# Optimization experiments

Hardware: AMD Instinct MI355X
Metric: run time of the kernel (lower is better)

The kernel has to match this reference:

```python
import jax, jax.numpy as jnp
import numpy as np

N_HEAD = 16

def setup_inputs() -> dict:
    key = jax.random.key(0)
    k1, k2, k3 = jax.random.split(key, 3)
    B, T, C = 2, 2048, 2048
    x = jax.random.normal(k1, (B, T, C), dtype=jnp.float32)
    # torch Linear weights are [out, in]; init with small scale for stability
    w_attn = jax.random.normal(k2, (3 * C, C), dtype=jnp.float32) * 0.02
    b_attn = jnp.zeros((3 * C,), dtype=jnp.float32)
    w_proj = jax.random.normal(k3, (C, C), dtype=jnp.float32) * 0.02
    b_proj = jnp.zeros((C,), dtype=jnp.float32)
    return {"x": x, "w_attn": w_attn, "b_attn": b_attn, "w_proj": w_proj, "b_proj": b_proj}

def reference(x, w_attn, b_attn, w_proj, b_proj):
    B, T, C = x.shape
    nh = N_HEAD
    hs = C // nh
    # fused QKV projection (torch Linear: x @ W^T + b)
    qkv = x @ w_attn.T + b_attn                      # [B, T, 3C]
    q, k, v = jnp.split(qkv, 3, axis=2)
    # [B, nh, T, hs]
    q = q.reshape(B, T, nh, hs).transpose(0, 2, 1, 3)
    k = k.reshape(B, T, nh, hs).transpose(0, 2, 1, 3)
    v = v.reshape(B, T, nh, hs).transpose(0, 2, 1, 3)
    # causal scaled dot-product attention
    scale = 1.0 / jnp.sqrt(jnp.asarray(hs, dtype=x.dtype))
    logits = jnp.einsum("bhqd,bhkd->bhqk", q, k) * scale  # [B, nh, T, T]
    causal = jnp.tril(jnp.ones((T, T), dtype=bool))
    logits = jnp.where(causal, logits, jnp.finfo(logits.dtype).min)
    attn = jax.nn.softmax(logits, axis=-1)
    y = jnp.einsum("bhqk,bhkd->bhqd", attn, v)       # [B, nh, T, hs]
    y = y.transpose(0, 2, 1, 3).reshape(B, T, C)
    # output projection (resid_dropout is identity in eval / p=0)
    y = y @ w_proj.T + b_proj
    return y
```

## Files before the change

### kernel.cpp

```cpp
#include <hip/hip_runtime.h>
#include <stdint.h>

typedef __bf16 bf16_t;
typedef __bf16 bf16x8 __attribute__((ext_vector_type(8)));
typedef float f32x4 __attribute__((ext_vector_type(4)));
typedef unsigned short us16x8 __attribute__((ext_vector_type(8)));

#define MFMA16(a, b, c) __builtin_amdgcn_mfma_f32_16x16x32_bf16(a, b, c, 0, 0, 0)
#define BAR() __builtin_amdgcn_s_barrier()
#define PRIO1() __builtin_amdgcn_s_setprio(1)
#define PRIO0() __builtin_amdgcn_s_setprio(0)
#define LGKM0()                                        \
  do {                                                 \
    asm volatile("s_waitcnt lgkmcnt(0)" ::: "memory"); \
    __builtin_amdgcn_sched_barrier(0);                 \
  } while (0)
#define VMCNT(n)                                          \
  do {                                                    \
    asm volatile("s_waitcnt vmcnt(" #n ")" ::: "memory"); \
    __builtin_amdgcn_sched_barrier(0);                    \
  } while (0)

__device__ __forceinline__ void stage16(const bf16_t* g, bf16_t* l) {
  __builtin_amdgcn_global_load_lds((__attribute__((address_space(1))) void*)g,
                                   (__attribute__((address_space(3))) void*)l, 16, 0, 0);
}

__global__ __launch_bounds__(256) void cvt_f32_to_bf16(const float* __restrict__ in,
                                                       bf16_t* __restrict__ out, int n8) {
  int i = blockIdx.x * 256 + threadIdx.x;
  if (i >= n8) return;
  const f32x4* p = (const f32x4*)(in + (size_t)i * 8);
  f32x4 a = p[0], b = p[1];
  bf16x8 o;
  o[0] = (bf16_t)a[0]; o[1] = (bf16_t)a[1]; o[2] = (bf16_t)a[2]; o[3] = (bf16_t)a[3];
  o[4] = (bf16_t)b[0]; o[5] = (bf16_t)b[1]; o[6] = (bf16_t)b[2]; o[7] = (bf16_t)b[3];
  *(bf16x8*)(out + (size_t)i * 8) = o;
}

template <int OUT_BF16>
__global__ __launch_bounds__(256, 2) void gemm_w128p(const bf16_t* __restrict__ A,
                                                     const bf16_t* __restrict__ B,
                                                     const float* __restrict__ bias,
                                                     void* __restrict__ Cout,
                                                     int M, int N, int K) {
  __shared__ bf16_t SA[3 * 256 * 32];
  __shared__ bf16_t SB[3 * 128 * 32];
  const int tid = threadIdx.x;
  const int l = tid & 63, w = tid >> 6;
  const int l15 = l & 15, l4 = l >> 4;
  const int wm = w >> 1, wn = w & 1;
  const int nbn = N >> 7;
  const int nbm = M >> 8;
  const int total = nbm * nbn;
  const int bnpc = nbn >> 3;

  const int r0 = tid >> 2;
  const int scol = (((tid & 3) ^ ((r0 >> 1) & 3)) << 3);
  const size_t K64 = (size_t)64 * K;

  const int swz = (l4 ^ ((l15 >> 1) & 3)) << 3;
  int aoff[8], boff[4];
#pragma unroll
  for (int i = 0; i < 8; ++i) aoff[i] = (wm * 128 + i * 16 + l15) * 32 + swz;
#pragma unroll
  for (int i = 0; i < 4; ++i) boff[i] = (wn * 64 + i * 16 + l15) * 32 + swz;

  const int nk = K >> 5;

  for (int wk = blockIdx.x; wk < total; wk += gridDim.x) {
    const int c = wk & 7, rr0 = wk >> 3;
    const int bm = rr0 / bnpc;
    const int bn = c * bnpc + rr0 % bnpc;

    const bf16_t* gA = A + (size_t)(bm * 256 + r0) * K + scol;
    const bf16_t* gB = B + (size_t)(bn * 128 + r0) * K + scol;

    f32x4 acc[8][4] = {};

    auto STAGE = [&](int t2, int buf) {
      const size_t ko = (size_t)t2 * 32;
      stage16(gA + ko, SA + buf * 8192 + tid * 8);
      stage16(gA + K64 + ko, SA + buf * 8192 + 2048 + tid * 8);
      stage16(gA + 2 * K64 + ko, SA + buf * 8192 + 4096 + tid * 8);
      stage16(gA + 3 * K64 + ko, SA + buf * 8192 + 6144 + tid * 8);
      stage16(gB + ko, SB + buf * 4096 + tid * 8);
      stage16(gB + K64 + ko, SB + buf * 4096 + 2048 + tid * 8);
    };

    auto TILE = [&](int t, int bufR, int bufS) {
      const int t2 = (t + 2 < nk) ? t + 2 : nk - 1;
      STAGE(t2, bufS);
      bf16x8 aR[8], bR[4];
#pragma unroll
      for (int i = 0; i < 8; ++i) aR[i] = *(const bf16x8*)(SA + bufR * 8192 + aoff[i]);
#pragma unroll
      for (int i = 0; i < 4; ++i) bR[i] = *(const bf16x8*)(SB + bufR * 4096 + boff[i]);
      VMCNT(6);
      BAR();
      LGKM0();
      PRIO1();
#pragma unroll
      for (int mi = 0; mi < 8; ++mi)
#pragma unroll
        for (int ni = 0; ni < 4; ++ni)
          acc[mi][ni] = MFMA16(aR[mi], bR[ni], acc[mi][ni]);
      PRIO0();
      BAR();
    };

    STAGE(0, 0);
    STAGE(1, 1);
    VMCNT(6);
    BAR();

    for (int t = 0; t < nk - 1; t += 3) {
      TILE(t, 0, 2);
      TILE(t + 1, 1, 0);
      TILE(t + 2, 2, 1);
    }
    TILE(nk - 1, 0, 2);
    VMCNT(0);

    const int rbase = bm * 256 + wm * 128 + (l4 << 2);
    const int cbase = bn * 128 + wn * 64 + l15;
#pragma unroll
    for (int ni = 0; ni < 4; ++ni) {
      float bv = bias[cbase + ni * 16];
#pragma unroll
      for (int mi = 0; mi < 8; ++mi)
#pragma unroll
        for (int rr = 0; rr < 4; ++rr) {
          float v = acc[mi][ni][rr] + bv;
          size_t off = (size_t)(rbase + mi * 16 + rr) * N + (cbase + ni * 16);
          if (OUT_BF16) ((bf16_t*)Cout)[off] = (bf16_t)v;
          else ((float*)Cout)[off] = v;
        }
    }
  }
}

template <int OUT_BF16>
__global__ __launch_bounds__(256, 3) void gemm_tb3(const bf16_t* __restrict__ A,
                                                   const bf16_t* __restrict__ B,
                                                   const float* __restrict__ bias,
                                                   void* __restrict__ Cout,
                                                   int M, int N, int K) {
  __shared__ bf16_t SA[3 * 128 * 32];
  __shared__ bf16_t SB[3 * 128 * 32];
  const int tid = threadIdx.x;
  const int l = tid & 63, w = tid >> 6;
  const int l15 = l & 15, l4 = l >> 4;
  const int wm = w >> 1, wn = w & 1;
  const int nbm = M >> 7;
  const int nwg = gridDim.x;
  const int bid = blockIdx.x;
  const int wg = (bid & 7) * (nwg >> 3) + (bid >> 3);
  const int bn = wg / nbm, bm = wg % nbm;

  const int r0 = tid >> 2;
  const int sc = (((tid & 3) ^ ((r0 >> 1) & 3)) << 3);
  const bf16_t* gA = A + (size_t)(bm * 128 + r0) * K + sc;
  const bf16_t* gB = B + (size_t)(bn * 128 + r0) * K + sc;
  const size_t rowK64 = (size_t)64 * K;

  const int swz = (l4 ^ ((l15 >> 1) & 3)) << 3;
  int aoff[4], boff[4];
#pragma unroll
  for (int i = 0; i < 4; ++i) {
    aoff[i] = (wm * 64 + i * 16 + l15) * 32 + swz;
    boff[i] = (wn * 64 + i * 16 + l15) * 32 + swz;
  }

  f32x4 acc[4][4] = {};
  const int nk = K >> 5;

  auto STAGE = [&](int t2, int buf) {
    const size_t ko = (size_t)t2 * 32;
    stage16(gA + ko, SA + buf * 4096 + tid * 8);
    stage16(gA + rowK64 + ko, SA + buf * 4096 + 2048 + tid * 8);
    stage16(gB + ko, SB + buf * 4096 + tid * 8);
    stage16(gB + rowK64 + ko, SB + buf * 4096 + 2048 + tid * 8);
  };

  auto TILE = [&](int t, int bufR, int bufS) {
    const int t2 = (t + 2 < nk) ? t + 2 : nk - 1;
    STAGE(t2, bufS);
    bf16x8 aR[4], bR[4];
#pragma unroll
    for (int i = 0; i < 4; ++i) {
      aR[i] = *(const bf16x8*)(SA + bufR * 4096 + aoff[i]);
      bR[i] = *(const bf16x8*)(SB + bufR * 4096 + boff[i]);
    }
    VMCNT(4);
    BAR();
    LGKM0();
    PRIO1();
#pragma unroll
    for (int mi = 0; mi < 4; ++mi)
#pragma unroll
      for (int ni = 0; ni < 4; ++ni)
        acc[mi][ni] = MFMA16(aR[mi], bR[ni], acc[mi][ni]);
    PRIO0();
    BAR();
  };

  STAGE(0, 0);
  STAGE(1, 1);
  VMCNT(4);
  BAR();

  for (int t = 0; t < nk - 1; t += 3) {
    TILE(t, 0, 2);
    TILE(t + 1, 1, 0);
    TILE(t + 2, 2, 1);
  }
  TILE(nk - 1, 0, 2);
  VMCNT(0);

  const int rbase = bm * 128 + wm * 64 + (l4 << 2);
  const int cbase = bn * 128 + wn * 64 + l15;
#pragma unroll
  for (int ni = 0; ni < 4; ++ni) {
    float bv = bias[cbase + ni * 16];
#pragma unroll
    for (int mi = 0; mi < 4; ++mi)
#pragma unroll
      for (int r = 0; r < 4; ++r) {
        float v = acc[mi][ni][r] + bv;
        size_t off = (size_t)(rbase + mi * 16 + r) * N + (cbase + ni * 16);
        if (OUT_BF16) ((bf16_t*)Cout)[off] = (bf16_t)v;
        else ((float*)Cout)[off] = v;
      }
  }
}

__global__ __launch_bounds__(256, 2) void attn_fwd(const bf16_t* __restrict__ qkv,
                                                   bf16_t* __restrict__ att) {
  __shared__ bf16_t Kt[64 * 128];
  __shared__ bf16_t Vt[128 * 64];
  __shared__ bf16_t Pw[4][16 * 64];

  int bid = blockIdx.x;
  int pair = bid >> 5, bh = bid & 31;
  int h = bh & 15, b = bh >> 4;
  int tid = threadIdx.x;
  int l = tid & 63, w = tid >> 6;
  int l15 = l & 15, l4 = l >> 4, l7 = l & 7;
  const size_t LD = 6144;
  const bf16_t* base = qkv + (size_t)b * 2048 * LD;

#pragma unroll 1
  for (int phase = 0; phase < 2; ++phase) {
    int qt = phase ? 31 - pair : pair;
    int q0 = qt << 6;
    int wq0 = q0 + w * 16;

    bf16x8 qf[4];
#pragma unroll
    for (int kk = 0; kk < 4; ++kk)
      qf[kk] = *(const bf16x8*)(base + (size_t)(wq0 + l15) * LD + h * 128 + kk * 32 + l4 * 8);

    f32x4 acc[8] = {};
    float mrow[4], lrow[4];
#pragma unroll
    for (int r = 0; r < 4; ++r) { mrow[r] = -1e30f; lrow[r] = 0.f; }

    int nkt = qt + 1;
    for (int kt = 0; kt < nkt; ++kt) {
      int kb = kt << 6;
      const bf16_t* vg = base + (size_t)kb * LD + 4096 + h * 128;
      us16x8 va[2], vb[2];
#pragma unroll
      for (int p = 0; p < 2; ++p) {
        int g = p * 256 + tid;
        int kv = (g >> 4) << 1;
        int d0 = (g & 15) << 3;
        va[p] = *(const us16x8*)(vg + (size_t)kv * LD + d0);
        vb[p] = *(const us16x8*)(vg + (size_t)(kv + 1) * LD + d0);
      }
      const bf16_t* kg = base + (size_t)kb * LD + 2048 + h * 128;
#pragma unroll
      for (int i = 0; i < 4; ++i) {
        int e = i * 256 + tid;
        int row = e >> 4, blk = e & 15;
        int src = (blk ^ (row & 7)) << 3;
        stage16(kg + (size_t)row * LD + src, Kt + e * 8);
      }
#pragma unroll
      for (int p = 0; p < 2; ++p) {
        int g = p * 256 + tid;
        int kv = (g >> 4) << 1;
        int d0 = (g & 15) << 3;
        int k8 = kv >> 3, kr = kv & 7;
#pragma unroll
        for (int j = 0; j < 8; ++j) {
          int d = d0 + j;
          int swz = k8 ^ ((d ^ (d >> 3)) & 7);
          unsigned pack = (unsigned)va[p][j] | ((unsigned)vb[p][j] << 16);
          *(unsigned*)(&Vt[d * 64 + swz * 8 + kr]) = pack;
        }
      }
      __syncthreads();

      {
        f32x4 s[4] = {};
        __builtin_amdgcn_s_setprio(1);
#pragma unroll
        for (int kk = 0; kk < 4; ++kk) {
          int blk = (kk * 4 + l4) ^ l7;
#pragma unroll
          for (int n = 0; n < 4; ++n) {
            bf16x8 kf = *(const bf16x8*)(Kt + (n * 16 + l15) * 128 + blk * 8);
            s[n] = MFMA16(qf[kk], kf, s[n]);
          }
        }
        __builtin_amdgcn_s_setprio(0);

        const float sc = 0.08838834764831845f;
        bool needMask = (kb + 63) > wq0;
        float scf[4];
#pragma unroll
        for (int r = 0; r < 4; ++r) {
          int q = wq0 + (l4 << 2) + r;
#pragma unroll
          for (int n = 0; n < 4; ++n) {
            float v = s[n][r] * sc;
            if (needMask && (kb + n * 16 + l15) > q) v = -1e30f;
            s[n][r] = v;
          }
          float mx = fmaxf(fmaxf(s[0][r], s[1][r]), fmaxf(s[2][r], s[3][r]));
          mx = fmaxf(mx, __shfl_xor(mx, 1));
          mx = fmaxf(mx, __shfl_xor(mx, 2));
          mx = fmaxf(mx, __shfl_xor(mx, 4));
          mx = fmaxf(mx, __shfl_xor(mx, 8));
          float mn = fmaxf(mrow[r], mx);
          float sf = __expf(mrow[r] - mn);
          mrow[r] = mn;
          scf[r] = sf;
          float rs = 0.f;
#pragma unroll
          for (int n = 0; n < 4; ++n) {
            float pv = __expf(s[n][r] - mn);
            s[n][r] = pv;
            rs += pv;
          }
          rs += __shfl_xor(rs, 1);
          rs += __shfl_xor(rs, 2);
          rs += __shfl_xor(rs, 4);
          rs += __shfl_xor(rs, 8);
          lrow[r] = lrow[r] * sf + rs;
        }
#pragma unroll
        for (int nd = 0; nd < 8; ++nd)
#pragma unroll
          for (int r = 0; r < 4; ++r)
            acc[nd][r] *= scf[r];
#pragma unroll
        for (int n = 0; n < 4; ++n) {
          int cb8 = n * 2 + (l15 >> 3);
#pragma unroll
          for (int r = 0; r < 4; ++r) {
            int row = (l4 << 2) + r;
            Pw[w][row * 64 + ((cb8 ^ (row & 7)) << 3) + l7] = (bf16_t)s[n][r];
          }
        }
        __builtin_amdgcn_s_setprio(1);
#pragma unroll
        for (int kk2 = 0; kk2 < 2; ++kk2) {
          bf16x8 pa = *(const bf16x8*)(&Pw[w][l15 * 64 + (((kk2 * 4 + l4) ^ l7) << 3)]);
#pragma unroll
          for (int nd = 0; nd < 8; ++nd) {
            int d = nd * 16 + l15;
            int swz = (kk2 * 4 + l4) ^ ((d ^ (d >> 3)) & 7);
            bf16x8 bv = *(const bf16x8*)(&Vt[d * 64 + swz * 8]);
            acc[nd] = MFMA16(pa, bv, acc[nd]);
          }
        }
        __builtin_amdgcn_s_setprio(0);
      }
      __syncthreads();
    }

#pragma unroll
    for (int r = 0; r < 4; ++r) {
      float inv = 1.0f / lrow[r];
      size_t ro = (size_t)(b * 2048 + wq0 + (l4 << 2) + r) * 2048 + h * 128;
#pragma unroll
      for (int nd = 0; nd < 8; ++nd)
        att[ro + nd * 16 + l15] = (bf16_t)(acc[nd][r] * inv);
    }
  }
}

extern "C" void kernel_launch(void* const* d_in, const int* in_sizes, int n_in,
                              void* d_out, int out_size, void* d_ws, size_t ws_size,
                              hipStream_t stream) {
  (void)in_sizes; (void)n_in; (void)out_size; (void)ws_size;
  const float* x = (const float*)d_in[0];
  const float* w_attn = (const float*)d_in[1];
  const float* b_attn = (const float*)d_in[2];
  const float* w_proj = (const float*)d_in[3];
  const float* b_proj = (const float*)d_in[4];
  float* out = (float*)d_out;

  char* ws = (char*)d_ws;
  bf16_t* xb  = (bf16_t*)(ws);
  bf16_t* wab = (bf16_t*)(ws + 16777216);
  bf16_t* wpb = (bf16_t*)(ws + 41943040);
  bf16_t* qkv = (bf16_t*)(ws + 50331648);
  bf16_t* att = xb;

  cvt_f32_to_bf16<<<4096, 256, 0, stream>>>(x, xb, 1048576);
  cvt_f32_to_bf16<<<6144, 256, 0, stream>>>(w_attn, wab, 1572864);
  cvt_f32_to_bf16<<<2048, 256, 0, stream>>>(w_proj, wpb, 524288);

  gemm_w128p<1><<<512, 256, 0, stream>>>(xb, wab, b_attn, qkv, 4096, 6144, 2048);

  attn_fwd<<<512, 256, 0, stream>>>(qkv, att);

  gemm_tb3<0><<<512, 256, 0, stream>>>(att, wpb, b_proj, out, 4096, 2048, 2048);
}
```

Baseline: 286.7 us.

## Double-buffer K/V tiles in attention, merge conversions, reuse wide GEMM for projection

Attention now double-buffers the K and V shared-memory tiles. The next tile's global loads are issued before the current tile's QK and PV math, which hides load latency and leaves one barrier per iteration. The three f32-to-bf16 conversion launches are merged into one kernel. The output projection now uses the 256x128-tile GEMM with 256 blocks instead of the removed 128x128 kernel. Doubling the K/V buffers raises LDS use and may cut attention occupancy, and the projection GEMM with 256 blocks may underfill the GPU.

New measurement: 296.9 us. 1.04x slower.

```diff
diff --git a/kernel.cpp b/kernel.cpp
--- a/kernel.cpp
+++ b/kernel.cpp
@@ -26,16 +26,33 @@
                                    (__attribute__((address_space(3))) void*)l, 16, 0, 0);
 }
 
-__global__ __launch_bounds__(256) void cvt_f32_to_bf16(const float* __restrict__ in,
-                                                       bf16_t* __restrict__ out, int n8) {
+__global__ __launch_bounds__(256) void cvt_all(const float* __restrict__ x,
+                                               const float* __restrict__ wa,
+                                               const float* __restrict__ wp,
+                                               bf16_t* __restrict__ xb,
+                                               bf16_t* __restrict__ wab,
+                                               bf16_t* __restrict__ wpb) {
   int i = blockIdx.x * 256 + threadIdx.x;
-  if (i >= n8) return;
-  const f32x4* p = (const f32x4*)(in + (size_t)i * 8);
+  const float* src;
+  bf16_t* dst;
+  if (i < 1048576) {
+    src = x + (size_t)i * 8;
+    dst = xb + (size_t)i * 8;
+  } else if (i < 2621440) {
+    size_t j = (size_t)(i - 1048576) * 8;
+    src = wa + j;
+    dst = wab + j;
+  } else {
+    size_t j = (size_t)(i - 2621440) * 8;
+    src = wp + j;
+    dst = wpb + j;
+  }
+  const f32x4* p = (const f32x4*)src;
   f32x4 a = p[0], b = p[1];
   bf16x8 o;
   o[0] = (bf16_t)a[0]; o[1] = (bf16_t)a[1]; o[2] = (bf16_t)a[2]; o[3] = (bf16_t)a[3];
   o[4] = (bf16_t)b[0]; o[5] = (bf16_t)b[1]; o[6] = (bf16_t)b[2]; o[7] = (bf16_t)b[3];
-  *(bf16x8*)(out + (size_t)i * 8) = o;
+  *(bf16x8*)dst = o;
 }
 
 template <int OUT_BF16>
@@ -140,105 +157,10 @@
   }
 }
 
-template <int OUT_BF16>
-__global__ __launch_bounds__(256, 3) void gemm_tb3(const bf16_t* __restrict__ A,
-                                                   const bf16_t* __restrict__ B,
-                                                   const float* __restrict__ bias,
-                                                   void* __restrict__ Cout,
-                                                   int M, int N, int K) {
-  __shared__ bf16_t SA[3 * 128 * 32];
-  __shared__ bf16_t SB[3 * 128 * 32];
-  const int tid = threadIdx.x;
-  const int l = tid & 63, w = tid >> 6;
-  const int l15 = l & 15, l4 = l >> 4;
-  const int wm = w >> 1, wn = w & 1;
-  const int nbm = M >> 7;
-  const int nwg = gridDim.x;
-  const int bid = blockIdx.x;
-  const int wg = (bid & 7) * (nwg >> 3) + (bid >> 3);
-  const int bn = wg / nbm, bm = wg % nbm;
-
-  const int r0 = tid >> 2;
-  const int sc = (((tid & 3) ^ ((r0 >> 1) & 3)) << 3);
-  const bf16_t* gA = A + (size_t)(bm * 128 + r0) * K + sc;
-  const bf16_t* gB = B + (size_t)(bn * 128 + r0) * K + sc;
-  const size_t rowK64 = (size_t)64 * K;
-
-  const int swz = (l4 ^ ((l15 >> 1) & 3)) << 3;
-  int aoff[4], boff[4];
-#pragma unroll
-  for (int i = 0; i < 4; ++i) {
-    aoff[i] = (wm * 64 + i * 16 + l15) * 32 + swz;
-    boff[i] = (wn * 64 + i * 16 + l15) * 32 + swz;
-  }
-
-  f32x4 acc[4][4] = {};
-  const int nk = K >> 5;
-
-  auto STAGE = [&](int t2, int buf) {
-    const size_t ko = (size_t)t2 * 32;
-    stage16(gA + ko, SA + buf * 4096 + tid * 8);
-    stage16(gA + rowK64 + ko, SA + buf * 4096 + 2048 + tid * 8);
-    stage16(gB + ko, SB + buf * 4096 + tid * 8);
-    stage16(gB + rowK64 + ko, SB + buf * 4096 + 2048 + tid * 8);
-  };
-
-  auto TILE = [&](int t, int bufR, int bufS) {
-    const int t2 = (t + 2 < nk) ? t + 2 : nk - 1;
-    STAGE(t2, bufS);
-    bf16x8 aR[4], bR[4];
-#pragma unroll
-    for (int i = 0; i < 4; ++i) {
-      aR[i] = *(const bf16x8*)(SA + bufR * 4096 + aoff[i]);
-      bR[i] = *(const bf16x8*)(SB + bufR * 4096 + boff[i]);
-    }
-    VMCNT(4);
-    BAR();
-    LGKM0();
-    PRIO1();
-#pragma unroll
-    for (int mi = 0; mi < 4; ++mi)
-#pragma unroll
-      for (int ni = 0; ni < 4; ++ni)
-        acc[mi][ni] = MFMA16(aR[mi], bR[ni], acc[mi][ni]);
-    PRIO0();
-    BAR();
-  };
-
-  STAGE(0, 0);
-  STAGE(1, 1);
-  VMCNT(4);
-  BAR();
-
-  for (int t = 0; t < nk - 1; t += 3) {
-    TILE(t, 0, 2);
-    TILE(t + 1, 1, 0);
-    TILE(t + 2, 2, 1);
-  }
-  TILE(nk - 1, 0, 2);
-  VMCNT(0);
-
-  const int rbase = bm * 128 + wm * 64 + (l4 << 2);
-  const int cbase = bn * 128 + wn * 64 + l15;
-#pragma unroll
-  for (int ni = 0; ni < 4; ++ni) {
-    float bv = bias[cbase + ni * 16];
-#pragma unroll
-    for (int mi = 0; mi < 4; ++mi)
-#pragma unroll
-      for (int r = 0; r < 4; ++r) {
-        float v = acc[mi][ni][r] + bv;
-        size_t off = (size_t)(rbase + mi * 16 + r) * N + (cbase + ni * 16);
-        if (OUT_BF16) ((bf16_t*)Cout)[off] = (bf16_t)v;
-        else ((float*)Cout)[off] = v;
-      }
-  }
-}
-
 __global__ __launch_bounds__(256, 2) void attn_fwd(const bf16_t* __restrict__ qkv,
                                                    bf16_t* __restrict__ att) {
-  __shared__ bf16_t Kt[64 * 128];
-  __shared__ bf16_t Vt[128 * 64];
+  __shared__ bf16_t Kt[2][64 * 128];
+  __shared__ bf16_t Vt[2][128 * 64];
   __shared__ bf16_t Pw[4][16 * 64];
 
   int bid = blockIdx.x;
@@ -250,6 +172,46 @@
   const size_t LD = 6144;
   const bf16_t* base = qkv + (size_t)b * 2048 * LD;
 
+  us16x8 va[2], vb[2];
+
+  auto loadV = [&](int kb) {
+    const bf16_t* vg = base + (size_t)kb * LD + 4096 + h * 128;
+#pragma unroll
+    for (int p = 0; p < 2; ++p) {
+      int g = p * 256 + tid;
+      int kvp = (g >> 4) << 1;
+      int d0 = (g & 15) << 3;
+      va[p] = *(const us16x8*)(vg + (size_t)kvp * LD + d0);
+      vb[p] = *(const us16x8*)(vg + (size_t)(kvp + 1) * LD + d0);
+    }
+  };
+  auto stageK = [&](int kb, int buf) {
+    const bf16_t* kg = base + (size_t)kb * LD + 2048 + h * 128;
+#pragma unroll
+    for (int i = 0; i < 4; ++i) {
+      int e = i * 256 + tid;
+      int row = e >> 4, blk = e & 15;
+      int src = (blk ^ (row & 7)) << 3;
+      stage16(kg + (size_t)row * LD + src, &Kt[buf][e * 8]);
+    }
+  };
+  auto writeV = [&](int buf) {
+#pragma unroll
+    for (int p = 0; p < 2; ++p) {
+      int g = p * 256 + tid;
+      int kvp = (g >> 4) << 1;
+      int d0 = (g & 15) << 3;
+      int k8 = kvp >> 3, kr = kvp & 7;
+#pragma unroll
+      for (int j = 0; j < 8; ++j) {
+        int d = d0 + j;
+        int swzv = k8 ^ ((d ^ (d >> 3)) & 7);
+        unsigned pack = (unsigned)va[p][j] | ((unsigned)vb[p][j] << 16);
+        *(unsigned*)(&Vt[buf][d * 64 + swzv * 8 + kr]) = pack;
+      }
+    }
+  };
+
 #pragma unroll 1
   for (int phase = 0; phase < 2; ++phase) {
     int qt = phase ? 31 - pair : pair;
@@ -267,119 +229,110 @@
     for (int r = 0; r < 4; ++r) { mrow[r] = -1e30f; lrow[r] = 0.f; }
 
     int nkt = qt + 1;
+
+    loadV(0);
+    stageK(0, 0);
+    VMCNT(4);
+    writeV(0);
+    LGKM0();
+    VMCNT(0);
+    BAR();
+
+#pragma unroll 1
     for (int kt = 0; kt < nkt; ++kt) {
-      int kb = kt << 6;
-      const bf16_t* vg = base + (size_t)kb * LD + 4096 + h * 128;
-      us16x8 va[2], vb[2];
-#pragma unroll
-      for (int p = 0; p < 2; ++p) {
-        int g = p * 256 + tid;
-        int kv = (g >> 4) << 1;
-        int d0 = (g & 15) << 3;
-        va[p] = *(const us16x8*)(vg + (size_t)kv * LD + d0);
-        vb[p] = *(const us16x8*)(vg + (size_t)(kv + 1) * LD + d0);
-      }
-      const bf16_t* kg = base + (size_t)kb * LD + 2048 + h * 128;
-#pragma unroll
-      for (int i = 0; i < 4; ++i) {
-        int e = i * 256 + tid;
-        int row = e >> 4, blk = e & 15;
-        int src = (blk ^ (row & 7)) << 3;
-        stage16(kg + (size_t)row * LD + src, Kt + e * 8);
-      }
-#pragma unroll
-      for (int p = 0; p < 2; ++p) {
-        int g = p * 256 + tid;
-        int kv = (g >> 4) << 1;
-        int d0 = (g & 15) << 3;
-        int k8 = kv >> 3, kr = kv & 7;
-#pragma unroll
-        for (int j = 0; j < 8; ++j) {
-          int d = d0 + j;
-          int swz = k8 ^ ((d ^ (d >> 3)) & 7);
-          unsigned pack = (unsigned)va[p][j] | ((unsigned)vb[p][j] << 16);
-          *(unsigned*)(&Vt[d * 64 + swz * 8 + kr]) = pack;
-        }
-      }
-      __syncthreads();
-
-      {
-        f32x4 s[4] = {};
-        __builtin_amdgcn_s_setprio(1);
-#pragma unroll
-        for (int kk = 0; kk < 4; ++kk) {
-          int blk = (kk * 4 + l4) ^ l7;
-#pragma unroll
-          for (int n = 0; n < 4; ++n) {
-            bf16x8 kf = *(const bf16x8*)(Kt + (n * 16 + l15) * 128 + blk * 8);
-            s[n] = MFMA16(qf[kk], kf, s[n]);
-          }
-        }
-        __builtin_amdgcn_s_setprio(0);
-
-        const float sc = 0.08838834764831845f;
-        bool needMask = (kb + 63) > wq0;
-        float scf[4];
+      const int cur = kt & 1, nxt = cur ^ 1;
+      const bool pf = (kt + 1 < nkt);
+      const int kb = kt << 6;
+      if (pf) {
+        loadV((kt + 1) << 6);
+        stageK((kt + 1) << 6, nxt);
+      }
+
+      f32x4 s[4] = {};
+      PRIO1();
+#pragma unroll
+      for (int kk = 0; kk < 4; ++kk) {
+        int blk = (kk * 4 + l4) ^ l7;
+#pragma unroll
+        for (int n = 0; n < 4; ++n) {
+          bf16x8 kf = *(const bf16x8*)(&Kt[cur][(n * 16 + l15) * 128 + blk * 8]);
+          s[n] = MFMA16(qf[kk], kf, s[n]);
+        }
+      }
+      PRIO0();
+
+      const float sc = 0.08838834764831845f;
+      bool needMask = (kb + 63) > wq0;
+      float scf[4];
+#pragma unroll
+      for (int r = 0; r < 4; ++r) {
+        int q = wq0 + (l4 << 2) + r;
+#pragma unroll
+        for (int n = 0; n < 4; ++n) {
+          float v = s[n][r] * sc;
+          if (needMask && (kb + n * 16 + l15) > q) v = -1e30f;
+          s[n][r] = v;
+        }
+        float mx = fmaxf(fmaxf(s[0][r], s[1][r]), fmaxf(s[2][r], s[3][r]));
+        mx = fmaxf(mx, __shfl_xor(mx, 1));
+        mx = fmaxf(mx, __shfl_xor(mx, 2));
+        mx = fmaxf(mx, __shfl_xor(mx, 4));
+        mx = fmaxf(mx, __shfl_xor(mx, 8));
+        float mn = fmaxf(mrow[r], mx);
+        float sf = __expf(mrow[r] - mn);
+        mrow[r] = mn;
+        scf[r] = sf;
+        float rs = 0.f;
+#pragma unroll
+        for (int n = 0; n < 4; ++n) {
+          float pv = __expf(s[n][r] - mn);
+          s[n][r] = pv;
+          rs += pv;
+        }
+        rs += __shfl_xor(rs, 1);
+        rs += __shfl_xor(rs, 2);
+        rs += __shfl_xor(rs, 4);
+        rs += __shfl_xor(rs, 8);
+        lrow[r] = lrow[r] * sf + rs;
+      }
+
+      if (pf) {
+        VMCNT(4);
+        writeV(nxt);
+      }
+
+#pragma unroll
+      for (int nd = 0; nd < 8; ++nd)
+#pragma unroll
+        for (int r = 0; r < 4; ++r)
+          acc[nd][r] *= scf[r];
+#pragma unroll
+      for (int n = 0; n < 4; ++n) {
+        int cb8 = n * 2 + (l15 >> 3);
 #pragma unroll
         for (int r = 0; r < 4; ++r) {
-          int q = wq0 + (l4 << 2) + r;
-#pragma unroll
-          for (int n = 0; n < 4; ++n) {
-            float v = s[n][r] * sc;
-            if (needMask && (kb + n * 16 + l15) > q) v = -1e30f;
-            s[n][r] = v;
-          }
-          float mx = fmaxf(fmaxf(s[0][r], s[1][r]), fmaxf(s[2][r], s[3][r]));
-          mx = fmaxf(mx, __shfl_xor(mx, 1));
-          mx = fmaxf(mx, __shfl_xor(mx, 2));
-          mx = fmaxf(mx, __shfl_xor(mx, 4));
-          mx = fmaxf(mx, __shfl_xor(mx, 8));
-          float mn = fmaxf(mrow[r], mx);
-          float sf = __expf(mrow[r] - mn);
-          mrow[r] = mn;
-          scf[r] = sf;
-          float rs = 0.f;
-#pragma unroll
-          for (int n = 0; n < 4; ++n) {
-            float pv = __expf(s[n][r] - mn);
-            s[n][r] = pv;
-            rs += pv;
-          }
-          rs += __shfl_xor(rs, 1);
-          rs += __shfl_xor(rs, 2);
-          rs += __shfl_xor(rs, 4);
-          rs += __shfl_xor(rs, 8);
-          lrow[r] = lrow[r] * sf + rs;
-        }
-#pragma unroll
-        for (int nd = 0; nd < 8; ++nd)
-#pragma unroll
-          for (int r = 0; r < 4; ++r)
-            acc[nd][r] *= scf[r];
-#pragma unroll
-        for (int n = 0; n < 4; ++n) {
-          int cb8 = n * 2 + (l15 >> 3);
-#pragma unroll
-          for (int r = 0; r < 4; ++r) {
-            int row = (l4 << 2) + r;
-            Pw[w][row * 64 + ((cb8 ^ (row & 7)) << 3) + l7] = (bf16_t)s[n][r];
-          }
-        }
-        __builtin_amdgcn_s_setprio(1);
-#pragma unroll
-        for (int kk2 = 0; kk2 < 2; ++kk2) {
-          bf16x8 pa = *(const bf16x8*)(&Pw[w][l15 * 64 + (((kk2 * 4 + l4) ^ l7) << 3)]);
-#pragma unroll
-          for (int nd = 0; nd < 8; ++nd) {
-            int d = nd * 16 + l15;
-            int swz = (kk2 * 4 + l4) ^ ((d ^ (d >> 3)) & 7);
-            bf16x8 bv = *(const bf16x8*)(&Vt[d * 64 + swz * 8]);
-            acc[nd] = MFMA16(pa, bv, acc[nd]);
-          }
-        }
-        __builtin_amdgcn_s_setprio(0);
-      }
-      __syncthreads();
+          int row = (l4 << 2) + r;
+          Pw[w][row * 64 + ((cb8 ^ (row & 7)) << 3) + l7] = (bf16_t)s[n][r];
+        }
+      }
+
+      PRIO1();
+#pragma unroll
+      for (int kk2 = 0; kk2 < 2; ++kk2) {
+        bf16x8 pa = *(const bf16x8*)(&Pw[w][l15 * 64 + (((kk2 * 4 + l4) ^ l7) << 3)]);
+#pragma unroll
+        for (int nd = 0; nd < 8; ++nd) {
+          int d = nd * 16 + l15;
+          int swzv = (kk2 * 4 + l4) ^ ((d ^ (d >> 3)) & 7);
+          bf16x8 bv = *(const bf16x8*)(&Vt[cur][d * 64 + swzv * 8]);
+          acc[nd] = MFMA16(pa, bv, acc[nd]);
+        }
+      }
+      PRIO0();
+
+      LGKM0();
+      VMCNT(0);
+      BAR();
     }
 
 #pragma unroll
@@ -411,13 +364,11 @@
   bf16_t* qkv = (bf16_t*)(ws + 50331648);
   bf16_t* att = xb;
 
-  cvt_f32_to_bf16<<<4096, 256, 0, stream>>>(x, xb, 1048576);
-  cvt_f32_to_bf16<<<6144, 256, 0, stream>>>(w_attn, wab, 1572864);
-  cvt_f32_to_bf16<<<2048, 256, 0, stream>>>(w_proj, wpb, 524288);
+  cvt_all<<<12288, 256, 0, stream>>>(x, w_attn, w_proj, xb, wab, wpb);
 
   gemm_w128p<1><<<512, 256, 0, stream>>>(xb, wab, b_attn, qkv, 4096, 6144, 2048);
 
   attn_fwd<<<512, 256, 0, stream>>>(qkv, att);
 
-  gemm_tb3<0><<<512, 256, 0, stream>>>(att, wpb, b_proj, out, 4096, 2048, 2048);
-}
+  gemm_w128p<0><<<256, 256, 0, stream>>>(att, wpb, b_proj, out, 4096, 2048, 2048);
+}
```
